# Optimization experiments

Measured on AMD Instinct MI355X. Metric: run time of the kernel, lower is better.

The kernel has to match this reference:

```python
import jax, jax.numpy as jnp
import numpy as np

# Poincare ball, curvature c = 1. Assumed manifold ops (standard hyperbolic-attention
# formulations, matching the hypll-style API used by the module):
#   HLinear(x)                ~ expmap0(logmap0(x) @ W + b)   (tangent-space linear)
#   attention_similarity      ~ (-d_poincare(q,k))/tau + gamma
#   attention_activation      ~ softmax over keys
#   attention_midpoint        ~ Mobius gyromidpoint: 0.5 (x) [sum_k w lam(v) v / sum_k w (lam(v)-1)]
#   cat                       ~ expmap0(concat(logmap0(heads)))

EPS = 1e-6
MAX_TANH_ARG = 1.0 - 1e-5

def _norm(x):
    return jnp.sqrt(jnp.clip(jnp.sum(x * x, axis=-1, keepdims=True), EPS))

def expmap0(v):
    n = _norm(v)
    return jnp.tanh(n) * v / n

def logmap0(x):
    n = _norm(x)
    return jnp.arctanh(jnp.minimum(n, MAX_TANH_ARG)) * x / n

def hlinear(x, W, b):
    return expmap0(logmap0(x) @ W + b)

def pairwise_poincare_dist(q, k):
    # q: [B,H,Sq,D] on ball, k: [B,Sk,D] on ball -> d: [B,H,Sq,Sk]
    qn = jnp.clip(jnp.sum(q * q, axis=-1), 0.0, 1.0 - 1e-5)            # [B,H,Sq]
    kn = jnp.clip(jnp.sum(k * k, axis=-1), 0.0, 1.0 - 1e-5)            # [B,Sk]
    dot = jnp.einsum('bhqd,bkd->bhqk', q, k)                            # GEMM-like
    sq = jnp.clip(qn[..., :, None] + kn[:, None, None, :] - 2.0 * dot, 0.0)
    denom = jnp.clip((1.0 - qn)[..., :, None] * (1.0 - kn)[:, None, None, :], EPS)
    arg = 1.0 + 2.0 * sq / denom
    return jnp.arccosh(jnp.maximum(arg, 1.0 + 1e-7))

def mobius_scalar_mul(r, x):
    n = _norm(x)
    return jnp.tanh(r * jnp.arctanh(jnp.minimum(n, MAX_TANH_ARG))) * x / n


def reference(query, key, value, Wq, bq, Wk, bk, Wv, bv, Wo, bo, scale_tau, scale_gamma):
    # batch_first=True; query/key/value: [B,S,D] points on the Poincare ball
    B, S, D = query.shape
    H = Wq.shape[0]

    # per-head full-dimension query projections, vectorized over heads
    tq = logmap0(query)                                                 # [B,S,D]
    q_h = expmap0(jnp.einsum('bsd,hde->bhse', tq, Wq) + bq[None, :, None, :])  # [B,H,S,D]
    # shared K/V projections (use_separate_kv_per_head=False -> MQA)
    k = hlinear(key, Wk, bk)                                            # [B,S,D]
    v = hlinear(value, Wv, bv)                                          # [B,S,D]

    tau = jnp.exp(-scale_tau[0])          # module passes tau = 1/exp(scale_tau)
    gamma = scale_gamma[0]

    d = pairwise_poincare_dist(q_h, k)                                  # [B,H,Sq,Sk]
    sim = -d / tau + gamma
    w = jax.nn.softmax(sim, axis=-1)                                    # [B,H,Sq,Sk]

    # Mobius gyromidpoint of values, weighted per query
    vn = jnp.clip(jnp.sum(v * v, axis=-1), 0.0, 1.0 - 1e-5)             # [B,Sk]
    lam = 2.0 / (1.0 - vn)                                              # [B,Sk]
    num = jnp.einsum('bhqk,bk,bkd->bhqd', w, lam, v)                    # [B,H,Sq,D]
    den = jnp.einsum('bhqk,bk->bhq', w, lam - 1.0)[..., None]           # [B,H,Sq,1]
    mid = mobius_scalar_mul(0.5, num / jnp.clip(den, EPS))              # [B,H,Sq,D]

    # manifold.cat: tangent-space concat of heads, back to the ball
    t = logmap0(mid)                                                    # [B,H,S,D]
    t = jnp.transpose(t, (0, 2, 1, 3)).reshape(B, S, H * D)             # [B,S,H*D]
    concat = expmap0(t)
    return hlinear(concat, Wo, bo)                                      # [B,S,D]


def setup_inputs() -> dict:
    key0 = jax.random.key(0)
    ks = jax.random.split(key0, 16)
    B, S, D, H = 4, 1024, 512, 8
    proj = lambda k: expmap0(0.02 * jax.random.normal(k, (B, S, D), dtype=jnp.float32))
    w_init = lambda k, shape, fan_in: (jax.random.normal(k, shape, dtype=jnp.float32) / np.sqrt(fan_in)).astype(jnp.float32)
    return {
        'query': proj(ks[0]),
        'key': proj(ks[1]),
        'value': proj(ks[2]),
        'Wq': w_init(ks[3], (H, D, D), D),
        'bq': 0.01 * jax.random.normal(ks[4], (H, D), dtype=jnp.float32),
        'Wk': w_init(ks[5], (D, D), D),
        'bk': 0.01 * jax.random.normal(ks[6], (D,), dtype=jnp.float32),
        'Wv': w_init(ks[7], (D, D), D),
        'bv': 0.01 * jax.random.normal(ks[8], (D,), dtype=jnp.float32),
        'Wo': w_init(ks[9], (H * D, D), H * D),
        'bo': 0.01 * jax.random.normal(ks[10], (D,), dtype=jnp.float32),
        'scale_tau': jnp.zeros((1,), dtype=jnp.float32),
        'scale_gamma': jnp.zeros((1,), dtype=jnp.float32),
    }
```

## Files before the change

### kernel.cpp

```cpp
#include <hip/hip_runtime.h>
#include <math.h>

constexpr int B_ = 4, S_ = 1024, D_ = 512, H_ = 8;
constexpr float EPS_ = 1e-6f;
constexpr float MAXT = 1.0f - 1e-5f;

typedef __attribute__((ext_vector_type(8))) short bf16x8;
typedef __attribute__((ext_vector_type(4))) float f32x4;

__device__ __forceinline__ ushort f2b(float f) {
    unsigned u = __float_as_uint(f);
    unsigned r = u + 0x7fffu + ((u >> 16) & 1u);
    return (ushort)(r >> 16);
}
__device__ __forceinline__ float b2f(ushort h) {
    return __uint_as_float(((unsigned)h) << 16);
}

__device__ __forceinline__ void async16(const ushort* g, ushort* l) {
    __builtin_amdgcn_global_load_lds(
        (const __attribute__((address_space(1))) unsigned int*)g,
        (__attribute__((address_space(3))) unsigned int*)l, 16, 0, 0);
}

__device__ __forceinline__ float blk_reduce_sum(float v, float* sm) {
    for (int o = 32; o > 0; o >>= 1) v += __shfl_down(v, o, 64);
    int lane = threadIdx.x & 63, wid = threadIdx.x >> 6;
    if (lane == 0) sm[wid] = v;
    __syncthreads();
    if (threadIdx.x == 0) sm[0] = sm[0] + sm[1] + sm[2] + sm[3];
    __syncthreads();
    float r = sm[0];
    __syncthreads();
    return r;
}

__device__ __forceinline__ void gemm_core256(const ushort* __restrict__ A,
                                             const ushort* __restrict__ B,
                                             int lda, int ldb, int K, int m0, int n0,
                                             ushort* As, ushort* Bs, f32x4 acc[4][8]) {
    const int tid = threadIdx.x;
    const int w = tid >> 6, lane = tid & 63;
    const int quad = lane >> 4, lx = lane & 15;
    const int rr = lane >> 2, c = lane & 3;

    const ushort* aP[4];
    ushort* lAp[4];
#pragma unroll
    for (int i = 0; i < 4; i++) {
        int r = w * 64 + i * 16 + rr;
        int q = c ^ ((r >> 1) & 3);
        aP[i] = A + (size_t)(m0 + r) * lda + q * 8;
        lAp[i] = As + (w * 64 + i * 16) * 32;
    }
    const ushort* bP[2];
    ushort* lBp[2];
#pragma unroll
    for (int i = 0; i < 2; i++) {
        int r = w * 32 + i * 16 + rr;
        int q = c ^ ((r >> 1) & 3);
        bP[i] = B + (size_t)(n0 + r) * ldb + q * 8;
        lBp[i] = Bs + (w * 32 + i * 16) * 32;
    }

    int raOff[4], rbOff[8];
#pragma unroll
    for (int i = 0; i < 4; i++) {
        int ra = w * 64 + i * 16 + lx;
        raOff[i] = ra * 32 + (quad ^ ((ra >> 1) & 3)) * 8;
    }
#pragma unroll
    for (int j = 0; j < 8; j++) {
        int rb = j * 16 + lx;
        rbOff[j] = rb * 32 + (quad ^ ((rb >> 1) & 3)) * 8;
    }
#pragma unroll
    for (int i = 0; i < 4; i++)
#pragma unroll
        for (int j = 0; j < 8; j++) acc[i][j] = (f32x4)(0.0f);

    for (int k0 = 0; k0 < K; k0 += 32) {
        __syncthreads();
        async16(aP[0] + k0, lAp[0]);
        async16(aP[1] + k0, lAp[1]);
        async16(aP[2] + k0, lAp[2]);
        async16(aP[3] + k0, lAp[3]);
        async16(bP[0] + k0, lBp[0]);
        async16(bP[1] + k0, lBp[1]);
        asm volatile("s_waitcnt vmcnt(0)" ::: "memory");
        __syncthreads();
        bf16x8 af[4], bfr[8];
#pragma unroll
        for (int i = 0; i < 4; i++) af[i] = *(const bf16x8*)(As + raOff[i]);
#pragma unroll
        for (int j = 0; j < 8; j++) bfr[j] = *(const bf16x8*)(Bs + rbOff[j]);
#pragma unroll
        for (int i = 0; i < 4; i++)
#pragma unroll
            for (int j = 0; j < 8; j++)
                acc[i][j] = __builtin_amdgcn_mfma_f32_16x16x32_bf16(af[i], bfr[j], acc[i][j], 0, 0, 0);
    }
}

__global__ __launch_bounds__(256, 2) void k_gemm_proj_all(const ushort* __restrict__ tq,
                                                          const ushort* __restrict__ tk,
                                                          const ushort* __restrict__ tv,
                                                          const ushort* __restrict__ WqT,
                                                          const ushort* __restrict__ WkT,
                                                          const ushort* __restrict__ WvT,
                                                          const float* __restrict__ bq,
                                                          const float* __restrict__ bk,
                                                          const float* __restrict__ bv,
                                                          float* __restrict__ yq,
                                                          float* __restrict__ yk,
                                                          float* __restrict__ yv) {
    __shared__ ushort As[256 * 32], Bs[128 * 32];
    int z = blockIdx.z;
    const ushort* A;
    const ushort* BT;
    const float* bias;
    float* C;
    int remap = 0, h = 0;
    if (z == 0) { A = tk; BT = WkT; bias = bk; C = yk; }
    else if (z == 1) { A = tv; BT = WvT; bias = bv; C = yv; }
    else {
        h = z - 2;
        A = tq; BT = WqT + (size_t)h * 512 * 512; bias = bq + (size_t)h * 512;
        C = yq; remap = 1;
    }
    f32x4 acc[4][8];
    int m0 = blockIdx.y * 256, n0 = blockIdx.x * 128;
    gemm_core256(A, BT, 512, 512, 512, m0, n0, As, Bs, acc);
    int tid = threadIdx.x, w = tid >> 6, lane = tid & 63;
    int quad = lane >> 4, lx = lane & 15;
#pragma unroll
    for (int i = 0; i < 4; i++)
#pragma unroll
        for (int reg = 0; reg < 4; reg++) {
            int m = m0 + w * 64 + i * 16 + quad * 4 + reg;
            size_t orow = remap ? (size_t)((m >> 10) * H_ + h) * S_ + (m & 1023) : (size_t)m;
#pragma unroll
            for (int j = 0; j < 8; j++) {
                int n = n0 + j * 16 + lx;
                C[orow * 512 + n] = acc[i][j][reg] + bias[n];
            }
        }
}

__global__ __launch_bounds__(256, 2) void k_gemm_score(const ushort* __restrict__ Aq,
                                                       const ushort* __restrict__ Bk,
                                                       ushort* __restrict__ E,
                                                       float* __restrict__ den,
                                                       const float* __restrict__ qn,
                                                       const float* __restrict__ kn,
                                                       const float* __restrict__ lamM1,
                                                       const float* __restrict__ stau) {
    __shared__ ushort As[256 * 32], Bs[128 * 32];
    int b = blockIdx.z;
    Aq += (size_t)b * 8192 * 512;
    Bk += (size_t)b * 1024 * 512;
    E += (size_t)b * 8192 * 1024;
    den += (size_t)b * 8192;
    qn += (size_t)b * 8192;
    kn += (size_t)b * 1024;
    lamM1 += (size_t)b * 1024;
    f32x4 acc[4][8];
    int m0 = blockIdx.y * 256, n0 = blockIdx.x * 128;
    gemm_core256(Aq, Bk, 512, 512, 512, m0, n0, As, Bs, acc);
    float itau = expf(stau[0]);
    int tid = threadIdx.x, w_ = tid >> 6, lane = tid & 63;
    int quad = lane >> 4, lx = lane & 15;
    float knv[8], okn[8], lmv[8];
#pragma unroll
    for (int j = 0; j < 8; j++) {
        int n = n0 + j * 16 + lx;
        knv[j] = kn[n];
        okn[j] = 1.0f - knv[j];
        lmv[j] = lamM1[n];
    }
#pragma unroll
    for (int i = 0; i < 4; i++)
#pragma unroll
        for (int reg = 0; reg < 4; reg++) {
            int m = m0 + w_ * 64 + i * 16 + quad * 4 + reg;
            float q = qn[m];
            float omq = 1.0f - q;
            float rsum = 0.0f;
#pragma unroll
            for (int j = 0; j < 8; j++) {
                float dot = acc[i][j][reg];
                float sq = fmaxf(q + knv[j] - 2.0f * dot, 0.0f);
                float dn = fmaxf(omq * okn[j], EPS_);
                float w = fmaxf(2.0f * sq * __builtin_amdgcn_rcpf(dn), 1e-7f);
                float root = __builtin_amdgcn_sqrtf(w * (w + 2.0f));
                float t = 1.0f + w + root;
                float e = __builtin_amdgcn_exp2f(-itau * __builtin_amdgcn_logf(t));
                ushort eb = f2b(e);
                int n = n0 + j * 16 + lx;
                E[(size_t)m * 1024 + n] = eb;
                rsum += b2f(eb) * lmv[j];
            }
            for (int o = 8; o; o >>= 1) rsum += __shfl_xor(rsum, o, 64);
            if (lx == 0) atomicAdd(&den[m], rsum);
        }
}

__global__ __launch_bounds__(256, 2) void k_gemm_attnv(const ushort* __restrict__ E,
                                                       const ushort* __restrict__ VT,
                                                       const float* __restrict__ den,
                                                       ushort* __restrict__ Ub,
                                                       float* __restrict__ ssU) {
    __shared__ ushort As[256 * 32], Bs[128 * 32];
    int b = blockIdx.z;
    E += (size_t)b * 8192 * 1024;
    VT += (size_t)b * 512 * 1024;
    den += (size_t)b * 8192;
    Ub += (size_t)b * 8192 * 512;
    ssU += (size_t)b * 8192;
    f32x4 acc[4][8];
    int m0 = blockIdx.y * 256, n0 = blockIdx.x * 128;
    gemm_core256(E, VT, 1024, 1024, 1024, m0, n0, As, Bs, acc);
    int tid = threadIdx.x, w = tid >> 6, lane = tid & 63;
    int quad = lane >> 4, lx = lane & 15;
#pragma unroll
    for (int i = 0; i < 4; i++)
#pragma unroll
        for (int reg = 0; reg < 4; reg++) {
            int m = m0 + w * 64 + i * 16 + quad * 4 + reg;
            float inv = 1.0f / fmaxf(den[m], EPS_);
            float ssum = 0.0f;
#pragma unroll
            for (int j = 0; j < 8; j++) {
                int n = n0 + j * 16 + lx;
                float u = acc[i][j][reg] * inv;
                Ub[(size_t)m * 512 + n] = f2b(u);
                ssum += u * u;
            }
            for (int o = 8; o; o >>= 1) ssum += __shfl_xor(ssum, o, 64);
            if (lx == 0) atomicAdd(&ssU[m], ssum);
        }
}

__global__ __launch_bounds__(256, 2) void k_gemm_sk(const ushort* __restrict__ Ub,
                                                    const ushort* __restrict__ WoT,
                                                    float* __restrict__ Cp) {
    __shared__ ushort As[256 * 32], Bs[128 * 32];
    int z = blockIdx.z;
    int m0 = blockIdx.y * 256, n0 = blockIdx.x * 128;
    int bb = m0 >> 10, s0 = m0 & 1023;
    const ushort* A = Ub + ((size_t)(bb * H_ + z) * S_ + s0) * 512;
    const ushort* BT = WoT + (size_t)z * 512;
    float* C = Cp + (size_t)z * 4096 * 512;
    f32x4 acc[4][8];
    gemm_core256(A, BT, 512, 4096, 512, 0, n0, As, Bs, acc);
    int tid = threadIdx.x, w = tid >> 6, lane = tid & 63;
    int quad = lane >> 4, lx = lane & 15;
#pragma unroll
    for (int i = 0; i < 4; i++)
#pragma unroll
        for (int reg = 0; reg < 4; reg++) {
            int m = m0 + w * 64 + i * 16 + quad * 4 + reg;
#pragma unroll
            for (int j = 0; j < 8; j++) {
                int n = n0 + j * 16 + lx;
                C[(size_t)m * 512 + n] = acc[i][j][reg];
            }
        }
}

__global__ __launch_bounds__(256) void k_hyperfactors(const float* __restrict__ ssU,
                                                      float* __restrict__ Asc8) {
    int idx = blockIdx.x * 256 + threadIdx.x;
    if (idx >= B_ * S_) return;
    int b = idx >> 10, s = idx & 1023;
    float f12[8];
    float sum = 0.0f;
#pragma unroll
    for (int h = 0; h < H_; h++) {
        float ss = ssU[(size_t)(b * H_ + h) * S_ + s];
        float n = sqrtf(fmaxf(ss, EPS_));
        float a = 0.5f * atanhf(fminf(n, MAXT));
        float f1 = tanhf(a) / n;
        float mss = f1 * f1 * ss;
        float nm = sqrtf(fmaxf(mss, EPS_));
        float f2 = atanhf(fminf(nm, MAXT)) / nm;
        f12[h] = f1 * f2;
        sum += f12[h] * f12[h] * ss;
    }
    float nc = sqrtf(fmaxf(sum, EPS_));
    float f3 = tanhf(nc) / nc;
    float css = f3 * f3 * sum;
    float nc2 = sqrtf(fmaxf(css, EPS_));
    float f4 = atanhf(fminf(nc2, MAXT)) / nc2;
    float g = f3 * f4;
#pragma unroll
    for (int h = 0; h < H_; h++) Asc8[(size_t)idx * 8 + h] = f12[h] * g;
}

__global__ __launch_bounds__(256) void k_final_reduce_expmap(const float* __restrict__ Cp,
                                                             const float* __restrict__ Asc8,
                                                             const float* __restrict__ bo,
                                                             float* __restrict__ out) {
    __shared__ float sm[8];
    int r = blockIdx.x;
    float a[8];
#pragma unroll
    for (int z = 0; z < 8; z++) a[z] = Asc8[(size_t)r * 8 + z];
    float v0 = bo[threadIdx.x], v1 = bo[threadIdx.x + 256];
#pragma unroll
    for (int z = 0; z < 8; z++) {
        const float* row = Cp + ((size_t)z * 4096 + r) * 512;
        v0 += a[z] * row[threadIdx.x];
        v1 += a[z] * row[threadIdx.x + 256];
    }
    float ss = blk_reduce_sum(v0 * v0 + v1 * v1, sm);
    float n = sqrtf(fmaxf(ss, EPS_));
    float f = tanhf(n) / n;
    float* o = out + (size_t)r * D_;
    o[threadIdx.x] = f * v0;
    o[threadIdx.x + 256] = f * v1;
}

__global__ __launch_bounds__(256) void k_logmap_bf16(const float* __restrict__ q,
                                                     const float* __restrict__ k,
                                                     const float* __restrict__ v,
                                                     ushort* __restrict__ tq,
                                                     ushort* __restrict__ tk,
                                                     ushort* __restrict__ tv) {
    __shared__ float sm[8];
    const float* x = (blockIdx.y == 0) ? q : (blockIdx.y == 1) ? k : v;
    ushort* t = (blockIdx.y == 0) ? tq : (blockIdx.y == 1) ? tk : tv;
    int r = blockIdx.x;
    const float* xr = x + (size_t)r * D_;
    float v0 = xr[threadIdx.x], v1 = xr[threadIdx.x + 256];
    float ss = blk_reduce_sum(v0 * v0 + v1 * v1, sm);
    float n = sqrtf(fmaxf(ss, EPS_));
    float f = atanhf(fminf(n, MAXT)) / n;
    ushort* tr = t + (size_t)r * D_;
    tr[threadIdx.x] = f2b(f * v0);
    tr[threadIdx.x + 256] = f2b(f * v1);
}

__global__ __launch_bounds__(256) void k_expmap_stats(const float* __restrict__ y,
                                                      float* __restrict__ outf,
                                                      ushort* __restrict__ outb,
                                                      float* __restrict__ aux, int mode) {
    __shared__ float sm[8];
    int r = blockIdx.x;
    const float* yr = y + (size_t)r * D_;
    float v0 = yr[threadIdx.x], v1 = yr[threadIdx.x + 256];
    float ss = blk_reduce_sum(v0 * v0 + v1 * v1, sm);
    float n = sqrtf(fmaxf(ss, EPS_));
    float f = tanhf(n) / n;
    ushort h0 = f2b(f * v0), h1 = f2b(f * v1);
    float x0 = b2f(h0), x1 = b2f(h1);
    float ss2 = blk_reduce_sum(x0 * x0 + x1 * x1, sm);
    float bn2 = fminf(ss2, MAXT);
    if (mode == 1) {
        ushort* o = outb + (size_t)r * D_;
        o[threadIdx.x] = h0;
        o[threadIdx.x + 256] = h1;
        if (threadIdx.x == 0) aux[r] = bn2;
    } else {
        float lam = 2.0f / (1.0f - bn2);
        float* o = outf + (size_t)r * D_;
        o[threadIdx.x] = lam * x0;
        o[threadIdx.x + 256] = lam * x1;
        if (threadIdx.x == 0) aux[r] = lam - 1.0f;
    }
}

__global__ __launch_bounds__(256) void k_transpose_f2b(const float* __restrict__ in,
                                                       ushort* __restrict__ out, int R, int C,
                                                       size_t zin, size_t zout) {
    __shared__ float t[32][33];
    in += (size_t)blockIdx.z * zin;
    out += (size_t)blockIdx.z * zout;
    int c0 = blockIdx.x * 32, r0 = blockIdx.y * 32;
    int tx = threadIdx.x & 31, ty = threadIdx.x >> 5;
    for (int rr = ty; rr < 32; rr += 8) t[rr][tx] = in[(size_t)(r0 + rr) * C + c0 + tx];
    __syncthreads();
    for (int rr = ty; rr < 32; rr += 8)
        out[(size_t)(c0 + rr) * R + r0 + tx] = f2b(t[tx][rr]);
}

extern "C" void kernel_launch(void* const* d_in, const int* in_sizes, int n_in,
                              void* d_out, int out_size, void* d_ws, size_t ws_size,
                              hipStream_t stream) {
    (void)in_sizes; (void)n_in; (void)out_size; (void)ws_size;
    const float* query = (const float*)d_in[0];
    const float* key = (const float*)d_in[1];
    const float* value = (const float*)d_in[2];
    const float* Wq = (const float*)d_in[3];
    const float* bq = (const float*)d_in[4];
    const float* Wk = (const float*)d_in[5];
    const float* bk = (const float*)d_in[6];
    const float* Wv = (const float*)d_in[7];
    const float* bv = (const float*)d_in[8];
    const float* Wo = (const float*)d_in[9];
    const float* bo = (const float*)d_in[10];
    const float* stau = (const float*)d_in[11];
    float* out = (float*)d_out;

    char* p = (char*)d_ws;
    auto alloc = [&](size_t bytes) {
        char* r = p;
        p += (bytes + 255) & ~(size_t)255;
        return r;
    };
    ushort* tq = (ushort*)alloc((size_t)4096 * 512 * 2);
    ushort* tk = (ushort*)alloc((size_t)4096 * 512 * 2);
    ushort* tv = (ushort*)alloc((size_t)4096 * 512 * 2);
    ushort* WqT = (ushort*)alloc((size_t)8 * 512 * 512 * 2);
    ushort* WkT = (ushort*)alloc((size_t)512 * 512 * 2);
    ushort* WvT = (ushort*)alloc((size_t)512 * 512 * 2);
    ushort* WoT = (ushort*)alloc((size_t)4096 * 512 * 2);
    float* yq = (float*)alloc((size_t)32768 * 512 * 4);
    float* yk = (float*)alloc((size_t)4096 * 512 * 4);
    float* yv = (float*)alloc((size_t)4096 * 512 * 4);
    ushort* qh = (ushort*)alloc((size_t)32768 * 512 * 2);
    ushort* kball = (ushort*)alloc((size_t)4096 * 512 * 2);
    float* lamv = (float*)alloc((size_t)4096 * 512 * 4);
    ushort* lamvT = (ushort*)alloc((size_t)4 * 512 * 1024 * 2);
    ushort* Sc = (ushort*)alloc((size_t)4 * 8192 * 1024 * 2);
    float* kn = (float*)alloc(4096 * 4);
    float* lamM1 = (float*)alloc(4096 * 4);
    float* qn = (float*)alloc(32768 * 4);
    float* den = (float*)alloc(32768 * 4);
    float* ssU = (float*)alloc(32768 * 4);
    float* Asc8 = (float*)alloc(32768 * 4);
    ushort* Ub = qh;
    float* Cp = (float*)Sc;

    hipMemsetAsync(den, 0, 2 * 32768 * 4, stream);

    k_logmap_bf16<<<dim3(4096, 3), 256, 0, stream>>>(query, key, value, tq, tk, tv);

    k_transpose_f2b<<<dim3(16, 16, 1), 256, 0, stream>>>(Wk, WkT, 512, 512, 0, 0);
    k_transpose_f2b<<<dim3(16, 16, 1), 256, 0, stream>>>(Wv, WvT, 512, 512, 0, 0);
    k_transpose_f2b<<<dim3(16, 16, 8), 256, 0, stream>>>(Wq, WqT, 512, 512, (size_t)512 * 512,
                                                         (size_t)512 * 512);
    k_transpose_f2b<<<dim3(16, 128, 1), 256, 0, stream>>>(Wo, WoT, 4096, 512, 0, 0);

    k_gemm_proj_all<<<dim3(4, 16, 10), 256, 0, stream>>>(tq, tk, tv, WqT, WkT, WvT, bq, bk, bv,
                                                         yq, yk, yv);

    k_expmap_stats<<<4096, 256, 0, stream>>>(yk, nullptr, kball, kn, 1);
    k_expmap_stats<<<4096, 256, 0, stream>>>(yv, lamv, nullptr, lamM1, 2);
    k_expmap_stats<<<32768, 256, 0, stream>>>(yq, nullptr, qh, qn, 1);
    k_transpose_f2b<<<dim3(16, 32, 4), 256, 0, stream>>>(lamv, lamvT, 1024, 512,
                                                         (size_t)1024 * 512, (size_t)512 * 1024);

    k_gemm_score<<<dim3(8, 32, 4), 256, 0, stream>>>(qh, kball, Sc, den, qn, kn, lamM1, stau);
    k_gemm_attnv<<<dim3(4, 32, 4), 256, 0, stream>>>(Sc, lamvT, den, Ub, ssU);

    k_hyperfactors<<<16, 256, 0, stream>>>(ssU, Asc8);

    k_gemm_sk<<<dim3(4, 16, 8), 256, 0, stream>>>(Ub, WoT, Cp);
    k_final_reduce_expmap<<<4096, 256, 0, stream>>>(Cp, Asc8, bo, out);
}
```

Baseline: 405.9 us.

## Double-buffer GEMM LDS loads, store projections in bf16, add tau==1 fast path

The shared GEMM core now double-buffers its LDS tiles, prefetching the next K-step with async global-to-LDS loads while MFMAs run on the current one. Projection outputs and the lambda-scaled value buffer are written as bf16 instead of fp32, which halves intermediate traffic, and a bf16 transpose replaces the float one. The score epilogue precomputes reciprocals and uses a plain reciprocal when exp(tau) is exactly 1, which is the default input. The costs are reduced precision before expmap and doubled LDS per block, which may lower occupancy.

```diff
diff --git a/kernel.cpp b/kernel.cpp
--- a/kernel.cpp
+++ b/kernel.cpp
@@ -35,32 +35,36 @@
     return r;
 }
 
+constexpr int GC_ABUF = 256 * 32;
+constexpr int GC_BUF = (256 + 128) * 32;
+constexpr int GC_SH = GC_BUF * 2;
+
 __device__ __forceinline__ void gemm_core256(const ushort* __restrict__ A,
                                              const ushort* __restrict__ B,
                                              int lda, int ldb, int K, int m0, int n0,
-                                             ushort* As, ushort* Bs, f32x4 acc[4][8]) {
+                                             ushort* __restrict__ sh, f32x4 acc[4][8]) {
     const int tid = threadIdx.x;
     const int w = tid >> 6, lane = tid & 63;
     const int quad = lane >> 4, lx = lane & 15;
     const int rr = lane >> 2, c = lane & 3;
 
     const ushort* aP[4];
-    ushort* lAp[4];
+    int aOff[4];
 #pragma unroll
     for (int i = 0; i < 4; i++) {
         int r = w * 64 + i * 16 + rr;
         int q = c ^ ((r >> 1) & 3);
         aP[i] = A + (size_t)(m0 + r) * lda + q * 8;
-        lAp[i] = As + (w * 64 + i * 16) * 32;
+        aOff[i] = (w * 64 + i * 16) * 32;
     }
     const ushort* bP[2];
-    ushort* lBp[2];
+    int bOff[2];
 #pragma unroll
     for (int i = 0; i < 2; i++) {
         int r = w * 32 + i * 16 + rr;
         int q = c ^ ((r >> 1) & 3);
         bP[i] = B + (size_t)(n0 + r) * ldb + q * 8;
-        lBp[i] = Bs + (w * 32 + i * 16) * 32;
+        bOff[i] = GC_ABUF + (w * 32 + i * 16) * 32;
     }
 
     int raOff[4], rbOff[8];
@@ -72,33 +76,45 @@
 #pragma unroll
     for (int j = 0; j < 8; j++) {
         int rb = j * 16 + lx;
-        rbOff[j] = rb * 32 + (quad ^ ((rb >> 1) & 3)) * 8;
+        rbOff[j] = GC_ABUF + rb * 32 + (quad ^ ((rb >> 1) & 3)) * 8;
     }
 #pragma unroll
     for (int i = 0; i < 4; i++)
 #pragma unroll
         for (int j = 0; j < 8; j++) acc[i][j] = (f32x4)(0.0f);
 
-    for (int k0 = 0; k0 < K; k0 += 32) {
-        __syncthreads();
-        async16(aP[0] + k0, lAp[0]);
-        async16(aP[1] + k0, lAp[1]);
-        async16(aP[2] + k0, lAp[2]);
-        async16(aP[3] + k0, lAp[3]);
-        async16(bP[0] + k0, lBp[0]);
-        async16(bP[1] + k0, lBp[1]);
-        asm volatile("s_waitcnt vmcnt(0)" ::: "memory");
-        __syncthreads();
+#pragma unroll
+    for (int i = 0; i < 4; i++) async16(aP[i], sh + aOff[i]);
+#pragma unroll
+    for (int i = 0; i < 2; i++) async16(bP[i], sh + bOff[i]);
+
+    const int nsteps = K >> 5;
+    for (int s = 0; s < nsteps; s++) {
+        ushort* cur = sh + (s & 1) * GC_BUF;
+        if (s + 1 < nsteps) {
+            ushort* nxt = sh + ((s + 1) & 1) * GC_BUF;
+            int k0 = (s + 1) << 5;
+#pragma unroll
+            for (int i = 0; i < 4; i++) async16(aP[i] + k0, nxt + aOff[i]);
+#pragma unroll
+            for (int i = 0; i < 2; i++) async16(bP[i] + k0, nxt + bOff[i]);
+            asm volatile("s_waitcnt vmcnt(6)" ::: "memory");
+        } else {
+            asm volatile("s_waitcnt vmcnt(0)" ::: "memory");
+        }
+        asm volatile("s_barrier" ::: "memory");
         bf16x8 af[4], bfr[8];
 #pragma unroll
-        for (int i = 0; i < 4; i++) af[i] = *(const bf16x8*)(As + raOff[i]);
-#pragma unroll
-        for (int j = 0; j < 8; j++) bfr[j] = *(const bf16x8*)(Bs + rbOff[j]);
+        for (int i = 0; i < 4; i++) af[i] = *(const bf16x8*)(cur + raOff[i]);
+#pragma unroll
+        for (int j = 0; j < 8; j++) bfr[j] = *(const bf16x8*)(cur + rbOff[j]);
 #pragma unroll
         for (int i = 0; i < 4; i++)
 #pragma unroll
             for (int j = 0; j < 8; j++)
                 acc[i][j] = __builtin_amdgcn_mfma_f32_16x16x32_bf16(af[i], bfr[j], acc[i][j], 0, 0, 0);
+        asm volatile("s_waitcnt lgkmcnt(0)" ::: "memory");
+        asm volatile("s_barrier" ::: "memory");
     }
 }
 
@@ -111,15 +127,15 @@
                                                           const float* __restrict__ bq,
                                                           const float* __restrict__ bk,
                                                           const float* __restrict__ bv,
-                                                          float* __restrict__ yq,
-                                                          float* __restrict__ yk,
-                                                          float* __restrict__ yv) {
-    __shared__ ushort As[256 * 32], Bs[128 * 32];
+                                                          ushort* __restrict__ yq,
+                                                          ushort* __restrict__ yk,
+                                                          ushort* __restrict__ yv) {
+    __shared__ ushort sh[GC_SH];
     int z = blockIdx.z;
     const ushort* A;
     const ushort* BT;
     const float* bias;
-    float* C;
+    ushort* C;
     int remap = 0, h = 0;
     if (z == 0) { A = tk; BT = WkT; bias = bk; C = yk; }
     else if (z == 1) { A = tv; BT = WvT; bias = bv; C = yv; }
@@ -130,7 +146,7 @@
     }
     f32x4 acc[4][8];
     int m0 = blockIdx.y * 256, n0 = blockIdx.x * 128;
-    gemm_core256(A, BT, 512, 512, 512, m0, n0, As, Bs, acc);
+    gemm_core256(A, BT, 512, 512, 512, m0, n0, sh, acc);
     int tid = threadIdx.x, w = tid >> 6, lane = tid & 63;
     int quad = lane >> 4, lx = lane & 15;
 #pragma unroll
@@ -142,7 +158,7 @@
 #pragma unroll
             for (int j = 0; j < 8; j++) {
                 int n = n0 + j * 16 + lx;
-                C[orow * 512 + n] = acc[i][j][reg] + bias[n];
+                C[orow * 512 + n] = f2b(acc[i][j][reg] + bias[n]);
             }
         }
 }
@@ -155,7 +171,7 @@
                                                        const float* __restrict__ kn,
                                                        const float* __restrict__ lamM1,
                                                        const float* __restrict__ stau) {
-    __shared__ ushort As[256 * 32], Bs[128 * 32];
+    __shared__ ushort sh[GC_SH];
     int b = blockIdx.z;
     Aq += (size_t)b * 8192 * 512;
     Bk += (size_t)b * 1024 * 512;
@@ -166,16 +182,17 @@
     lamM1 += (size_t)b * 1024;
     f32x4 acc[4][8];
     int m0 = blockIdx.y * 256, n0 = blockIdx.x * 128;
-    gemm_core256(Aq, Bk, 512, 512, 512, m0, n0, As, Bs, acc);
+    gemm_core256(Aq, Bk, 512, 512, 512, m0, n0, sh, acc);
     float itau = expf(stau[0]);
+    bool tau1 = (itau == 1.0f);
     int tid = threadIdx.x, w_ = tid >> 6, lane = tid & 63;
     int quad = lane >> 4, lx = lane & 15;
-    float knv[8], okn[8], lmv[8];
+    float knv[8], rk[8], lmv[8];
 #pragma unroll
     for (int j = 0; j < 8; j++) {
         int n = n0 + j * 16 + lx;
         knv[j] = kn[n];
-        okn[j] = 1.0f - knv[j];
+        rk[j] = __builtin_amdgcn_rcpf(1.0f - knv[j]);
         lmv[j] = lamM1[n];
     }
 #pragma unroll
@@ -184,17 +201,18 @@
         for (int reg = 0; reg < 4; reg++) {
             int m = m0 + w_ * 64 + i * 16 + quad * 4 + reg;
             float q = qn[m];
-            float omq = 1.0f - q;
+            float rq2 = 2.0f * __builtin_amdgcn_rcpf(1.0f - q);
             float rsum = 0.0f;
 #pragma unroll
             for (int j = 0; j < 8; j++) {
                 float dot = acc[i][j][reg];
                 float sq = fmaxf(q + knv[j] - 2.0f * dot, 0.0f);
-                float dn = fmaxf(omq * okn[j], EPS_);
-                float w = fmaxf(2.0f * sq * __builtin_amdgcn_rcpf(dn), 1e-7f);
-                float root = __builtin_amdgcn_sqrtf(w * (w + 2.0f));
+                float rr2 = fminf(rq2 * rk[j], 2e6f);
+                float w = fmaxf(sq * rr2, 1e-7f);
+                float root = __builtin_amdgcn_sqrtf(__builtin_fmaf(w, w, 2.0f * w));
                 float t = 1.0f + w + root;
-                float e = __builtin_amdgcn_exp2f(-itau * __builtin_amdgcn_logf(t));
+                float e = tau1 ? __builtin_amdgcn_rcpf(t)
+                               : __builtin_amdgcn_exp2f(-itau * __builtin_amdgcn_logf(t));
                 ushort eb = f2b(e);
                 int n = n0 + j * 16 + lx;
                 E[(size_t)m * 1024 + n] = eb;
@@ -210,7 +228,7 @@
                                                        const float* __restrict__ den,
                                                        ushort* __restrict__ Ub,
                                                        float* __restrict__ ssU) {
-    __shared__ ushort As[256 * 32], Bs[128 * 32];
+    __shared__ ushort sh[GC_SH];
     int b = blockIdx.z;
     E += (size_t)b * 8192 * 1024;
     VT += (size_t)b * 512 * 1024;
@@ -219,7 +237,7 @@
     ssU += (size_t)b * 8192;
     f32x4 acc[4][8];
     int m0 = blockIdx.y * 256, n0 = blockIdx.x * 128;
-    gemm_core256(E, VT, 1024, 1024, 1024, m0, n0, As, Bs, acc);
+    gemm_core256(E, VT, 1024, 1024, 1024, m0, n0, sh, acc);
     int tid = threadIdx.x, w = tid >> 6, lane = tid & 63;
     int quad = lane >> 4, lx = lane & 15;
 #pragma unroll
@@ -227,7 +245,7 @@
 #pragma unroll
         for (int reg = 0; reg < 4; reg++) {
             int m = m0 + w * 64 + i * 16 + quad * 4 + reg;
-            float inv = 1.0f / fmaxf(den[m], EPS_);
+            float inv = __builtin_amdgcn_rcpf(fmaxf(den[m], EPS_));
             float ssum = 0.0f;
 #pragma unroll
             for (int j = 0; j < 8; j++) {
@@ -244,7 +262,7 @@
 __global__ __launch_bounds__(256, 2) void k_gemm_sk(const ushort* __restrict__ Ub,
                                                     const ushort* __restrict__ WoT,
                                                     float* __restrict__ Cp) {
-    __shared__ ushort As[256 * 32], Bs[128 * 32];
+    __shared__ ushort sh[GC_SH];
     int z = blockIdx.z;
     int m0 = blockIdx.y * 256, n0 = blockIdx.x * 128;
     int bb = m0 >> 10, s0 = m0 & 1023;
@@ -252,7 +270,7 @@
     const ushort* BT = WoT + (size_t)z * 512;
     float* C = Cp + (size_t)z * 4096 * 512;
     f32x4 acc[4][8];
-    gemm_core256(A, BT, 512, 4096, 512, 0, n0, As, Bs, acc);
+    gemm_core256(A, BT, 512, 4096, 512, 0, n0, sh, acc);
     int tid = threadIdx.x, w = tid >> 6, lane = tid & 63;
     int quad = lane >> 4, lx = lane & 15;
 #pragma unroll
@@ -341,14 +359,13 @@
     tr[threadIdx.x + 256] = f2b(f * v1);
 }
 
-__global__ __launch_bounds__(256) void k_expmap_stats(const float* __restrict__ y,
-                                                      float* __restrict__ outf,
+__global__ __launch_bounds__(256) void k_expmap_stats(const ushort* __restrict__ y,
                                                       ushort* __restrict__ outb,
                                                       float* __restrict__ aux, int mode) {
     __shared__ float sm[8];
     int r = blockIdx.x;
-    const float* yr = y + (size_t)r * D_;
-    float v0 = yr[threadIdx.x], v1 = yr[threadIdx.x + 256];
+    const ushort* yr = y + (size_t)r * D_;
+    float v0 = b2f(yr[threadIdx.x]), v1 = b2f(yr[threadIdx.x + 256]);
     float ss = blk_reduce_sum(v0 * v0 + v1 * v1, sm);
     float n = sqrtf(fmaxf(ss, EPS_));
     float f = tanhf(n) / n;
@@ -356,16 +373,15 @@
     float x0 = b2f(h0), x1 = b2f(h1);
     float ss2 = blk_reduce_sum(x0 * x0 + x1 * x1, sm);
     float bn2 = fminf(ss2, MAXT);
+    ushort* o = outb + (size_t)r * D_;
     if (mode == 1) {
-        ushort* o = outb + (size_t)r * D_;
         o[threadIdx.x] = h0;
         o[threadIdx.x + 256] = h1;
         if (threadIdx.x == 0) aux[r] = bn2;
     } else {
         float lam = 2.0f / (1.0f - bn2);
-        float* o = outf + (size_t)r * D_;
-        o[threadIdx.x] = lam * x0;
-        o[threadIdx.x + 256] = lam * x1;
+        o[threadIdx.x] = f2b(lam * x0);
+        o[threadIdx.x + 256] = f2b(lam * x1);
         if (threadIdx.x == 0) aux[r] = lam - 1.0f;
     }
 }
@@ -382,6 +398,20 @@
     __syncthreads();
     for (int rr = ty; rr < 32; rr += 8)
         out[(size_t)(c0 + rr) * R + r0 + tx] = f2b(t[tx][rr]);
+}
+
+__global__ __launch_bounds__(256) void k_transpose_b2b(const ushort* __restrict__ in,
+                                                       ushort* __restrict__ out, int R, int C,
+                                                       size_t zin, size_t zout) {
+    __shared__ ushort t[32][34];
+    in += (size_t)blockIdx.z * zin;
+    out += (size_t)blockIdx.z * zout;
+    int c0 = blockIdx.x * 32, r0 = blockIdx.y * 32;
+    int tx = threadIdx.x & 31, ty = threadIdx.x >> 5;
+    for (int rr = ty; rr < 32; rr += 8) t[rr][tx] = in[(size_t)(r0 + rr) * C + c0 + tx];
+    __syncthreads();
+    for (int rr = ty; rr < 32; rr += 8)
+        out[(size_t)(c0 + rr) * R + r0 + tx] = t[tx][rr];
 }
 
 extern "C" void kernel_launch(void* const* d_in, const int* in_sizes, int n_in,
@@ -415,12 +445,12 @@
     ushort* WkT = (ushort*)alloc((size_t)512 * 512 * 2);
     ushort* WvT = (ushort*)alloc((size_t)512 * 512 * 2);
     ushort* WoT = (ushort*)alloc((size_t)4096 * 512 * 2);
-    float* yq = (float*)alloc((size_t)32768 * 512 * 4);
-    float* yk = (float*)alloc((size_t)4096 * 512 * 4);
-    float* yv = (float*)alloc((size_t)4096 * 512 * 4);
+    ushort* yq = (ushort*)alloc((size_t)32768 * 512 * 2);
+    ushort* yk = (ushort*)alloc((size_t)4096 * 512 * 2);
+    ushort* yv = (ushort*)alloc((size_t)4096 * 512 * 2);
     ushort* qh = (ushort*)alloc((size_t)32768 * 512 * 2);
     ushort* kball = (ushort*)alloc((size_t)4096 * 512 * 2);
-    float* lamv = (float*)alloc((size_t)4096 * 512 * 4);
+    ushort* lamv = (ushort*)alloc((size_t)4096 * 512 * 2);
     ushort* lamvT = (ushort*)alloc((size_t)4 * 512 * 1024 * 2);
     ushort* Sc = (ushort*)alloc((size_t)4 * 8192 * 1024 * 2);
     float* kn = (float*)alloc(4096 * 4);
@@ -445,10 +475,10 @@
     k_gemm_proj_all<<<dim3(4, 16, 10), 256, 0, stream>>>(tq, tk, tv, WqT, WkT, WvT, bq, bk, bv,
                                                          yq, yk, yv);
 
-    k_expmap_stats<<<4096, 256, 0, stream>>>(yk, nullptr, kball, kn, 1);
-    k_expmap_stats<<<4096, 256, 0, stream>>>(yv, lamv, nullptr, lamM1, 2);
-    k_expmap_stats<<<32768, 256, 0, stream>>>(yq, nullptr, qh, qn, 1);
-    k_transpose_f2b<<<dim3(16, 32, 4), 256, 0, stream>>>(lamv, lamvT, 1024, 512,
+    k_expmap_stats<<<4096, 256, 0, stream>>>(yk, kball, kn, 1);
+    k_expmap_stats<<<4096, 256, 0, stream>>>(yv, lamv, lamM1, 2);
+    k_expmap_stats<<<32768, 256, 0, stream>>>(yq, qh, qn, 1);
+    k_transpose_b2b<<<dim3(16, 32, 4), 256, 0, stream>>>(lamv, lamvT, 1024, 512,
                                                          (size_t)1024 * 512, (size_t)512 * 1024);
 
     k_gemm_score<<<dim3(8, 32, 4), 256, 0, stream>>>(qh, kball, Sc, den, qn, kn, lamM1, stau);
```

New measurement: 390.1 us. 1.04x faster.
